# Optimization experiments

Measured on AMD Instinct MI355X. Metric: run time of the kernel, lower is better.

## Reference

```python
import jax, jax.numpy as jnp
import numpy as np

B, N, F_IN, HID, OUT, NHEADS = 16, 1024, 64, 64, 64, 4
TAXI = 512        # get_Parameter('taxi_size') from the original repo (node split point)
ALPHA = 0.2       # LeakyReLU negative slope


def setup_inputs() -> dict:
    key = jax.random.key(0)
    ks = jax.random.split(key, 8)
    x = jax.random.normal(ks[0], (B, N, F_IN), dtype=jnp.float32)
    # multiplicative binary mask (mostly ones so softmax rows are well-conditioned)
    mask = (jax.random.uniform(ks[1], (N, N)) > 0.1).astype(jnp.float32)
    s_in = 1.0 / np.sqrt(F_IN)
    s_cat = 1.0 / np.sqrt(NHEADS * HID)
    W1 = jax.random.normal(ks[2], (NHEADS, F_IN, HID), jnp.float32) * s_in
    W2 = jax.random.normal(ks[3], (NHEADS, F_IN, HID), jnp.float32) * s_in
    a = jax.random.normal(ks[4], (NHEADS, 2 * HID), jnp.float32) * 0.1
    W1o = jax.random.normal(ks[5], (NHEADS * HID, OUT), jnp.float32) * s_cat
    W2o = jax.random.normal(ks[6], (NHEADS * HID, OUT), jnp.float32) * s_cat
    ao = jax.random.normal(ks[7], (2 * OUT,), jnp.float32) * 0.1
    return dict(x=x, mask=mask, W1=W1, W2=W2, a=a, W1o=W1o, W2o=W2o, ao=ao)


def _gat_layer(x, mask, W1, W2, a, out_dim):
    # x: [B,N,F]; W1,W2: [F,out_dim]; a: [2*out_dim]
    # node-group-split linear projection (taxi nodes via W1, rest via W2)
    h = jnp.concatenate([x[:, :TAXI] @ W1, x[:, TAXI:] @ W2], axis=1)  # [B,N,O]
    A1 = h @ a[:out_dim]                 # [B,N]
    A2 = h @ a[out_dim:]                 # [B,N]
    sim = A1[:, :, None] + A2[:, None, :]  # [B,N,N] additive scores
    e = jax.nn.leaky_relu(sim, ALPHA)
    e = mask[None, :, :] * e             # multiplicative mask (as in source)
    attn = jax.nn.softmax(e, axis=-1)    # [B,N,N]  (dropout omitted: eval mode)
    h_prime = jnp.einsum('bnm,bmo->bno', attn, h)
    return jax.nn.elu(h_prime), attn


def reference(x, mask, W1, W2, a, W1o, W2o, ao):
    # input dropout omitted (eval mode)
    heads = [_gat_layer(x, mask, W1[i], W2[i], a[i], HID)[0] for i in range(NHEADS)]
    xc = jnp.concatenate(heads, axis=-1)          # [B,N,NHEADS*HID]
    out, attn = _gat_layer(xc, mask, W1o, W2o, ao, OUT)
    return out, attn
```

## Files before the change

kernel.cpp:

```cpp
#include <hip/hip_runtime.h>
#include <hip/hip_bf16.h>

#define B_      16
#define N_      1024
#define ALPHA_  0.2f

typedef __attribute__((ext_vector_type(8))) __bf16 bf16x8;
typedef __attribute__((ext_vector_type(4))) float  floatx4;

__device__ __forceinline__ float eluf(float u) { return u > 0.f ? u : __expf(u) - 1.f; }

__device__ __forceinline__ floatx4 mfma_bf16(bf16x8 a, bf16x8 b, floatx4 c) {
    return __builtin_amdgcn_mfma_f32_16x16x32_bf16(a, b, c, 0, 0, 0);
}

__device__ __forceinline__ void t_quad(const float4 a2v, const float4 ep, const float4 en,
                                       const float4 mv, const float th,
                                       const float e1p, const float e1n,
                                       float& z, float* o)
{
    float t0 = ((a2v.x > th) ? ep.x : en.x) * ((a2v.x > th) ? e1p : e1n);
    float t1 = ((a2v.y > th) ? ep.y : en.y) * ((a2v.y > th) ? e1p : e1n);
    float t2 = ((a2v.z > th) ? ep.z : en.z) * ((a2v.z > th) ? e1p : e1n);
    float t3 = ((a2v.w > th) ? ep.w : en.w) * ((a2v.w > th) ? e1p : e1n);
    t0 = (mv.x != 0.f) ? t0 : 1.f;
    t1 = (mv.y != 0.f) ? t1 : 1.f;
    t2 = (mv.z != 0.f) ? t2 : 1.f;
    t3 = (mv.w != 0.f) ? t3 : 1.f;
    z += ((t0 + t1) + (t2 + t3));
    o[0] = t0; o[1] = t1; o[2] = t2; o[3] = t3;
}

__global__ __launch_bounds__(256) void proj1_kernel(
    const float* __restrict__ x, const float* __restrict__ W1,
    const float* __restrict__ W2, const float* __restrict__ av,
    __bf16* __restrict__ h1t, float* __restrict__ A1, float* __restrict__ A2)
{
    const int tile = blockIdx.x, b = blockIdx.y, head = blockIdx.z;
    const int n0 = tile * 64;
    const float* W  = ((n0 < 512) ? W1 : W2) + head * 64 * 64;
    const float* ah = av + head * 128;

    __shared__ __align__(16) float xs[64][65];
    __shared__ __align__(16) float Wl[64][64];
    __shared__ __align__(16) float as_[128];

    const int tid = threadIdx.x;
    for (int i = 0; i < 16; ++i) {
        int idx = i * 256 + tid;
        int r = idx >> 6, f = idx & 63;
        xs[r][f] = x[(size_t)(b * N_ + n0 + r) * 64 + f];
        Wl[r][f] = W[idx];
    }
    if (tid < 128) as_[tid] = ah[tid];
    __syncthreads();

    const int r = tid >> 2, c0 = (tid & 3) * 16;
    float acc[16];
#pragma unroll
    for (int j = 0; j < 16; ++j) acc[j] = 0.f;
#pragma unroll 8
    for (int f = 0; f < 64; ++f) {
        float xv = xs[r][f];
#pragma unroll
        for (int j = 0; j < 16; ++j) acc[j] += xv * Wl[f][c0 + j];
    }

    float p1 = 0.f, p2 = 0.f;
#pragma unroll
    for (int j = 0; j < 16; ++j) {
        p1 += acc[j] * as_[c0 + j];
        p2 += acc[j] * as_[64 + c0 + j];
    }
    p1 += __shfl_xor(p1, 1); p1 += __shfl_xor(p1, 2);
    p2 += __shfl_xor(p2, 1); p2 += __shfl_xor(p2, 2);
    const int bh = head * B_ + b;
    if ((tid & 3) == 0) {
        A1[bh * N_ + n0 + r] = p1;
        A2[bh * N_ + n0 + r] = p2;
    }

    __syncthreads();
#pragma unroll
    for (int j = 0; j < 16; ++j) xs[r][c0 + j] = acc[j];
    __syncthreads();
    const int d = tid & 63, ch = tid >> 6;
    bf16x8 q0, q1;
#pragma unroll
    for (int j = 0; j < 8; ++j) q0[j] = (__bf16)xs[ch * 16 + j][d];
#pragma unroll
    for (int j = 0; j < 8; ++j) q1[j] = (__bf16)xs[ch * 16 + 8 + j][d];
    bf16x8* dst = (bf16x8*)(h1t + ((size_t)bh * 64 + d) * N_ + n0 + ch * 16);
    dst[0] = q0; dst[1] = q1;
}

__global__ __launch_bounds__(256, 4) void attn1_kernel(
    const float* __restrict__ A1g, const float* __restrict__ A2g,
    const __bf16* __restrict__ Htg, const float* __restrict__ maskg,
    __bf16* __restrict__ xc_out)
{
    const int tile = blockIdx.x, b = blockIdx.y, head = blockIdx.z;
    const int n0 = tile * 64;
    const int bh = head * B_ + b;
    const float* A1 = A1g + (size_t)bh * N_;
    const float* A2 = A2g + (size_t)bh * N_;
    const __bf16* Hglob = Htg + (size_t)bh * 64 * N_;

    __shared__ __align__(16) __bf16 ts[64][72];
    __shared__ __align__(16) __bf16 Ht[64][72];
    __shared__ __align__(16) float E2p[N_], E2n[N_], A2s[N_];
    __shared__ float invz[64];

    const int tid = threadIdx.x;
#pragma unroll
    for (int i = 0; i < 4; ++i) {
        int m = i * 256 + tid;
        float a2 = A2[m];
        A2s[m] = a2; E2p[m] = __expf(a2); E2n[m] = __expf(ALPHA_ * a2);
    }

    const int r = tid >> 2, q = tid & 3;
    const float a1r = A1[n0 + r];
    const float e1p = __expf(a1r), e1n = __expf(ALPHA_ * a1r), th = -a1r;
    const int w = tid >> 6, L = tid & 63, quad = L >> 4, lo = L & 15;

    floatx4 acc[4] = {{0,0,0,0},{0,0,0,0},{0,0,0,0},{0,0,0,0}};
    float zacc = 0.f;

    const float* mrow = maskg + (size_t)(n0 + r) * N_ + q * 16;
    const __bf16* hrow = Hglob + (size_t)r * N_ + q * 16;
    float4 pm0 = *(const float4*)(mrow);
    float4 pm1 = *(const float4*)(mrow + 4);
    float4 pm2 = *(const float4*)(mrow + 8);
    float4 pm3 = *(const float4*)(mrow + 12);
    bf16x8 ph0 = *(const bf16x8*)(hrow);
    bf16x8 ph1 = *(const bf16x8*)(hrow + 8);

    for (int mt = 0; mt < 16; ++mt) {
        float4 cm0 = pm0, cm1 = pm1, cm2 = pm2, cm3 = pm3;
        bf16x8 ch0 = ph0, ch1 = ph1;
        if (mt < 15) {
            const float* mnx = mrow + (mt + 1) * 64;
            const __bf16* hnx = hrow + (mt + 1) * 64;
            pm0 = *(const float4*)(mnx);      pm1 = *(const float4*)(mnx + 4);
            pm2 = *(const float4*)(mnx + 8);  pm3 = *(const float4*)(mnx + 12);
            ph0 = *(const bf16x8*)(hnx);      ph1 = *(const bf16x8*)(hnx + 8);
        }
        __syncthreads();
        const int mb = mt * 64 + q * 16;
        float o[16];
        t_quad(*(const float4*)&A2s[mb+0],  *(const float4*)&E2p[mb+0],  *(const float4*)&E2n[mb+0],  cm0, th, e1p, e1n, zacc, o+0);
        t_quad(*(const float4*)&A2s[mb+4],  *(const float4*)&E2p[mb+4],  *(const float4*)&E2n[mb+4],  cm1, th, e1p, e1n, zacc, o+4);
        t_quad(*(const float4*)&A2s[mb+8],  *(const float4*)&E2p[mb+8],  *(const float4*)&E2n[mb+8],  cm2, th, e1p, e1n, zacc, o+8);
        t_quad(*(const float4*)&A2s[mb+12], *(const float4*)&E2p[mb+12], *(const float4*)&E2n[mb+12], cm3, th, e1p, e1n, zacc, o+12);
        bf16x8 pk0 = {(__bf16)o[0], (__bf16)o[1], (__bf16)o[2], (__bf16)o[3],
                      (__bf16)o[4], (__bf16)o[5], (__bf16)o[6], (__bf16)o[7]};
        bf16x8 pk1 = {(__bf16)o[8], (__bf16)o[9], (__bf16)o[10], (__bf16)o[11],
                      (__bf16)o[12], (__bf16)o[13], (__bf16)o[14], (__bf16)o[15]};
        *(bf16x8*)&ts[r][q * 16]     = pk0;
        *(bf16x8*)&ts[r][q * 16 + 8] = pk1;
        *(bf16x8*)&Ht[r][q * 16]     = ch0;
        *(bf16x8*)&Ht[r][q * 16 + 8] = ch1;
        __syncthreads();
#pragma unroll
        for (int c = 0; c < 2; ++c) {
            bf16x8 af = *(bf16x8*)&ts[16 * w + lo][c * 32 + quad * 8];
#pragma unroll
            for (int t = 0; t < 4; ++t) {
                bf16x8 bv = *(bf16x8*)&Ht[16 * t + lo][c * 32 + quad * 8];
                acc[t] = mfma_bf16(af, bv, acc[t]);
            }
        }
    }

    zacc += __shfl_xor(zacc, 1);
    zacc += __shfl_xor(zacc, 2);
    if (q == 0) invz[r] = 1.f / zacc;
    __syncthreads();

#pragma unroll
    for (int t = 0; t < 4; ++t)
#pragma unroll
        for (int i = 0; i < 4; ++i) {
            const int n = 16 * w + quad * 4 + i;
            ts[n][16 * t + lo] = (__bf16)eluf(acc[t][i] * invz[n]);
        }
    __syncthreads();
#pragma unroll
    for (int i = 0; i < 2; ++i) {
        int cid = i * 256 + tid;
        int row = cid >> 3, c8 = (cid & 7) * 8;
        bf16x8 v = *(bf16x8*)&ts[row][c8];
        *(bf16x8*)(xc_out + ((size_t)(b * N_ + n0 + row)) * 256 + head * 64 + c8) = v;
    }
}

__global__ __launch_bounds__(256) void attn2_kernel(
    const float* __restrict__ A1g, const float* __restrict__ A2g,
    const __bf16* __restrict__ Htg, const float* __restrict__ maskg,
    float* __restrict__ out_f, float* __restrict__ attn_f)
{
    const int tile = blockIdx.x, b = blockIdx.y;
    const int n0 = tile * 64;
    const float* A1 = A1g + (size_t)b * N_;
    const float* A2 = A2g + (size_t)b * N_;
    const __bf16* Hglob = Htg + (size_t)b * 64 * N_;

    __shared__ __align__(16) __bf16 ts[64][72];
    __shared__ __align__(16) __bf16 Ht[64][72];
    __shared__ __align__(16) float E2p[N_], E2n[N_], A2s[N_];
    __shared__ float invz[64], E1pl[64], E1nl[64], A1sl[64];

    const int tid = threadIdx.x;
#pragma unroll
    for (int i = 0; i < 4; ++i) {
        int m = i * 256 + tid;
        float a2 = A2[m];
        A2s[m] = a2; E2p[m] = __expf(a2); E2n[m] = __expf(ALPHA_ * a2);
    }

    const int r = tid >> 2, q = tid & 3;
    const float a1r = A1[n0 + r];
    const float e1p = __expf(a1r), e1n = __expf(ALPHA_ * a1r), th = -a1r;
    if (q == 0) { E1pl[r] = e1p; E1nl[r] = e1n; A1sl[r] = a1r; }
    const int w = tid >> 6, L = tid & 63, quad = L >> 4, lo = L & 15;

    floatx4 acc[4] = {{0,0,0,0},{0,0,0,0},{0,0,0,0},{0,0,0,0}};
    float zacc = 0.f;

    const float* mrow = maskg + (size_t)(n0 + r) * N_ + q * 16;
    const __bf16* hrow = Hglob + (size_t)r * N_ + q * 16;
    float4 pm0 = *(const float4*)(mrow);
    float4 pm1 = *(const float4*)(mrow + 4);
    float4 pm2 = *(const float4*)(mrow + 8);
    float4 pm3 = *(const float4*)(mrow + 12);
    bf16x8 ph0 = *(const bf16x8*)(hrow);
    bf16x8 ph1 = *(const bf16x8*)(hrow + 8);

    for (int mt = 0; mt < 16; ++mt) {
        float4 cm0 = pm0, cm1 = pm1, cm2 = pm2, cm3 = pm3;
        bf16x8 ch0 = ph0, ch1 = ph1;
        if (mt < 15) {
            const float* mnx = mrow + (mt + 1) * 64;
            const __bf16* hnx = hrow + (mt + 1) * 64;
            pm0 = *(const float4*)(mnx);      pm1 = *(const float4*)(mnx + 4);
            pm2 = *(const float4*)(mnx + 8);  pm3 = *(const float4*)(mnx + 12);
            ph0 = *(const bf16x8*)(hnx);      ph1 = *(const bf16x8*)(hnx + 8);
        }
        __syncthreads();
        const int mb = mt * 64 + q * 16;
        float o[16];
        t_quad(*(const float4*)&A2s[mb+0],  *(const float4*)&E2p[mb+0],  *(const float4*)&E2n[mb+0],  cm0, th, e1p, e1n, zacc, o+0);
        t_quad(*(const float4*)&A2s[mb+4],  *(const float4*)&E2p[mb+4],  *(const float4*)&E2n[mb+4],  cm1, th, e1p, e1n, zacc, o+4);
        t_quad(*(const float4*)&A2s[mb+8],  *(const float4*)&E2p[mb+8],  *(const float4*)&E2n[mb+8],  cm2, th, e1p, e1n, zacc, o+8);
        t_quad(*(const float4*)&A2s[mb+12], *(const float4*)&E2p[mb+12], *(const float4*)&E2n[mb+12], cm3, th, e1p, e1n, zacc, o+12);
        bf16x8 pk0 = {(__bf16)o[0], (__bf16)o[1], (__bf16)o[2], (__bf16)o[3],
                      (__bf16)o[4], (__bf16)o[5], (__bf16)o[6], (__bf16)o[7]};
        bf16x8 pk1 = {(__bf16)o[8], (__bf16)o[9], (__bf16)o[10], (__bf16)o[11],
                      (__bf16)o[12], (__bf16)o[13], (__bf16)o[14], (__bf16)o[15]};
        *(bf16x8*)&ts[r][q * 16]     = pk0;
        *(bf16x8*)&ts[r][q * 16 + 8] = pk1;
        *(bf16x8*)&Ht[r][q * 16]     = ch0;
        *(bf16x8*)&Ht[r][q * 16 + 8] = ch1;
        __syncthreads();
#pragma unroll
        for (int c = 0; c < 2; ++c) {
            bf16x8 af = *(bf16x8*)&ts[16 * w + lo][c * 32 + quad * 8];
#pragma unroll
            for (int t = 0; t < 4; ++t) {
                bf16x8 bv = *(bf16x8*)&Ht[16 * t + lo][c * 32 + quad * 8];
                acc[t] = mfma_bf16(af, bv, acc[t]);
            }
        }
    }

    zacc += __shfl_xor(zacc, 1);
    zacc += __shfl_xor(zacc, 2);
    if (q == 0) invz[r] = 1.f / zacc;
    __syncthreads();

#pragma unroll
    for (int t = 0; t < 4; ++t)
#pragma unroll
        for (int i = 0; i < 4; ++i) {
            const int n = 16 * w + quad * 4 + i;
            out_f[((size_t)(b * N_ + n0 + n)) * 64 + 16 * t + lo] = eluf(acc[t][i] * invz[n]);
        }

    const float4 a2v = *(const float4*)&A2s[tid * 4];
    const float4 epv = *(const float4*)&E2p[tid * 4];
    const float4 env = *(const float4*)&E2n[tid * 4];
#pragma unroll 2
    for (int i = 0; i < 64; ++i) {
        const float e1pr = E1pl[i], e1nr = E1nl[i], thr = -A1sl[i], iz = invz[i];
        float4 mv = *(const float4*)(maskg + (size_t)(n0 + i) * N_ + tid * 4);
        float4 res;
        res.x = ((mv.x != 0.f) ? ((a2v.x > thr) ? epv.x * e1pr : env.x * e1nr) : 1.f) * iz;
        res.y = ((mv.y != 0.f) ? ((a2v.y > thr) ? epv.y * e1pr : env.y * e1nr) : 1.f) * iz;
        res.z = ((mv.z != 0.f) ? ((a2v.z > thr) ? epv.z * e1pr : env.z * e1nr) : 1.f) * iz;
        res.w = ((mv.w != 0.f) ? ((a2v.w > thr) ? epv.w * e1pr : env.w * e1nr) : 1.f) * iz;
        *(float4*)(attn_f + ((size_t)(b * N_ + n0 + i)) * N_ + tid * 4) = res;
    }
}

__global__ __launch_bounds__(256) void proj2_kernel(
    const __bf16* __restrict__ xcb, const float* __restrict__ W1o,
    const float* __restrict__ W2o, const float* __restrict__ ao,
    __bf16* __restrict__ h2t, float* __restrict__ A1o, float* __restrict__ A2o)
{
    const int tile = blockIdx.x, b = blockIdx.y;
    const int n0 = tile * 64;
    const float* W = (n0 < 512) ? W1o : W2o;

    __shared__ __align__(16) __bf16 xs[64][264];
    __shared__ __align__(16) __bf16 Wt[64][264];
    __shared__ __align__(16) float as_[128];

    const int tid = threadIdx.x;
    if (tid < 128) as_[tid] = ao[tid];

#pragma unroll
    for (int i = 0; i < 8; ++i) {
        int idx = i * 256 + tid;
        int row = idx >> 5, c = (idx & 31) * 8;
        *(bf16x8*)&xs[row][c] =
            *(const bf16x8*)(xcb + ((size_t)(b * N_ + n0 + row)) * 256 + c);
    }
#pragma unroll
    for (int i = 0; i < 16; ++i) {
        int idx = i * 256 + tid;
        int k = idx >> 4, n4 = (idx & 15) * 4;
        float4 wv = *(const float4*)(W + (size_t)k * 64 + n4);
        Wt[n4 + 0][k] = (__bf16)wv.x;
        Wt[n4 + 1][k] = (__bf16)wv.y;
        Wt[n4 + 2][k] = (__bf16)wv.z;
        Wt[n4 + 3][k] = (__bf16)wv.w;
    }
    __syncthreads();

    const int w = tid >> 6, L = tid & 63, quad = L >> 4, lo = L & 15;
    floatx4 acc[4] = {{0,0,0,0},{0,0,0,0},{0,0,0,0},{0,0,0,0}};
#pragma unroll
    for (int kc = 0; kc < 8; ++kc) {
        bf16x8 af = *(bf16x8*)&xs[16 * w + lo][kc * 32 + quad * 8];
#pragma unroll
        for (int t = 0; t < 4; ++t) {
            bf16x8 bv = *(bf16x8*)&Wt[16 * t + lo][kc * 32 + quad * 8];
            acc[t] = mfma_bf16(af, bv, acc[t]);
        }
    }

    float p1[4] = {0, 0, 0, 0}, p2[4] = {0, 0, 0, 0};
#pragma unroll
    for (int t = 0; t < 4; ++t) {
        float a1w = as_[16 * t + lo], a2w = as_[64 + 16 * t + lo];
#pragma unroll
        for (int i = 0; i < 4; ++i) { p1[i] += acc[t][i] * a1w; p2[i] += acc[t][i] * a2w; }
    }
#pragma unroll
    for (int s = 1; s < 16; s <<= 1)
#pragma unroll
        for (int i = 0; i < 4; ++i) {
            p1[i] += __shfl_xor(p1[i], s);
            p2[i] += __shfl_xor(p2[i], s);
        }
    if (lo == 0) {
#pragma unroll
        for (int i = 0; i < 4; ++i) {
            int n = 16 * w + quad * 4 + i;
            A1o[b * N_ + n0 + n] = p1[i];
            A2o[b * N_ + n0 + n] = p2[i];
        }
    }

    __syncthreads();
#pragma unroll
    for (int t = 0; t < 4; ++t)
#pragma unroll
        for (int i = 0; i < 4; ++i)
            xs[16 * w + quad * 4 + i][16 * t + lo] = (__bf16)acc[t][i];
    __syncthreads();
    const int d = tid & 63, ch = tid >> 6;
    bf16x8 v0, v1;
#pragma unroll
    for (int j = 0; j < 8; ++j) v0[j] = xs[ch * 16 + j][d];
#pragma unroll
    for (int j = 0; j < 8; ++j) v1[j] = xs[ch * 16 + 8 + j][d];
    bf16x8* dst = (bf16x8*)(h2t + ((size_t)b * 64 + d) * N_ + n0 + ch * 16);
    dst[0] = v0; dst[1] = v1;
}

extern "C" void kernel_launch(void* const* d_in, const int* in_sizes, int n_in,
                              void* d_out, int out_size, void* d_ws, size_t ws_size,
                              hipStream_t stream)
{
    const float* x    = (const float*)d_in[0];
    const float* mask = (const float*)d_in[1];
    const float* W1   = (const float*)d_in[2];
    const float* W2   = (const float*)d_in[3];
    const float* a    = (const float*)d_in[4];
    const float* W1o  = (const float*)d_in[5];
    const float* W2o  = (const float*)d_in[6];
    const float* ao   = (const float*)d_in[7];

    float* out      = (float*)d_out;
    float* attn_out = out + (size_t)B_ * N_ * 64;

    float*  ws  = (float*)d_ws;
    float*  A1  = ws;
    float*  A2  = A1 + 65536;
    float*  A1o = A2 + 65536;
    float*  A2o = A1o + 16384;
    __bf16* h1t = (__bf16*)(A2o + 16384);
    __bf16* h2t = h1t + 4194304;
    __bf16* xcb = h2t + 1048576;

    proj1_kernel<<<dim3(16, 16, 4), 256, 0, stream>>>(x, W1, W2, a, h1t, A1, A2);
    attn1_kernel<<<dim3(16, 16, 4), 256, 0, stream>>>(A1, A2, h1t, mask, xcb);
    proj2_kernel<<<dim3(16, 16, 1), 256, 0, stream>>>(xcb, W1o, W2o, ao, h2t, A1o, A2o);
    attn2_kernel<<<dim3(16, 16, 1), 256, 0, stream>>>(A1o, A2o, h2t, mask, out, attn_out);
}
```

Measured before the change: 177.4 us.

## Use bf16 MFMA in proj1 and shrink attn2 row tiles for more blocks

proj1 now stages x and a transposed W in shared memory as bf16 and computes the projection with 16x16x32 bf16 MFMA instead of scalar fp32 FMAs. The A1/A2 attention logits are reduced across 16 lanes with shuffles. attn2 goes from 64-row tiles to 16-row tiles, launching 1024 blocks instead of 256 so the final layer and its attention-matrix write fill the GPU. The cost is reduced precision in the first projection and less reuse of the H tile per block in attn2.

```diff
diff --git a/kernel.cpp b/kernel.cpp
--- a/kernel.cpp
+++ b/kernel.cpp
@@ -6,6 +6,7 @@
 #define ALPHA_  0.2f
 
 typedef __attribute__((ext_vector_type(8))) __bf16 bf16x8;
+typedef __attribute__((ext_vector_type(4))) __bf16 bf16x4;
 typedef __attribute__((ext_vector_type(4))) float  floatx4;
 
 __device__ __forceinline__ float eluf(float u) { return u > 0.f ? u : __expf(u) - 1.f; }
@@ -41,57 +42,76 @@
     const float* W  = ((n0 < 512) ? W1 : W2) + head * 64 * 64;
     const float* ah = av + head * 128;
 
-    __shared__ __align__(16) float xs[64][65];
-    __shared__ __align__(16) float Wl[64][64];
+    __shared__ __align__(16) __bf16 xs[64][72];
+    __shared__ __align__(16) __bf16 Wt[64][72];
     __shared__ __align__(16) float as_[128];
 
     const int tid = threadIdx.x;
-    for (int i = 0; i < 16; ++i) {
+    if (tid < 128) as_[tid] = ah[tid];
+#pragma unroll
+    for (int i = 0; i < 4; ++i) {
         int idx = i * 256 + tid;
-        int r = idx >> 6, f = idx & 63;
-        xs[r][f] = x[(size_t)(b * N_ + n0 + r) * 64 + f];
-        Wl[r][f] = W[idx];
-    }
-    if (tid < 128) as_[tid] = ah[tid];
-    __syncthreads();
-
-    const int r = tid >> 2, c0 = (tid & 3) * 16;
-    float acc[16];
-#pragma unroll
-    for (int j = 0; j < 16; ++j) acc[j] = 0.f;
-#pragma unroll 8
-    for (int f = 0; f < 64; ++f) {
-        float xv = xs[r][f];
-#pragma unroll
-        for (int j = 0; j < 16; ++j) acc[j] += xv * Wl[f][c0 + j];
-    }
-
-    float p1 = 0.f, p2 = 0.f;
-#pragma unroll
-    for (int j = 0; j < 16; ++j) {
-        p1 += acc[j] * as_[c0 + j];
-        p2 += acc[j] * as_[64 + c0 + j];
-    }
-    p1 += __shfl_xor(p1, 1); p1 += __shfl_xor(p1, 2);
-    p2 += __shfl_xor(p2, 1); p2 += __shfl_xor(p2, 2);
+        int r = idx >> 4, c = (idx & 15) * 4;
+        float4 v = *(const float4*)(x + ((size_t)(b * N_ + n0 + r)) * 64 + c);
+        xs[r][c+0] = (__bf16)v.x; xs[r][c+1] = (__bf16)v.y;
+        xs[r][c+2] = (__bf16)v.z; xs[r][c+3] = (__bf16)v.w;
+        float4 wv = *(const float4*)(W + (size_t)r * 64 + c);
+        Wt[c+0][r] = (__bf16)wv.x; Wt[c+1][r] = (__bf16)wv.y;
+        Wt[c+2][r] = (__bf16)wv.z; Wt[c+3][r] = (__bf16)wv.w;
+    }
+    __syncthreads();
+
+    const int w = tid >> 6, L = tid & 63, quad = L >> 4, lo = L & 15;
+    floatx4 acc[4] = {{0,0,0,0},{0,0,0,0},{0,0,0,0},{0,0,0,0}};
+#pragma unroll
+    for (int kc = 0; kc < 2; ++kc) {
+        bf16x8 af = *(bf16x8*)&xs[16 * w + lo][kc * 32 + quad * 8];
+#pragma unroll
+        for (int t = 0; t < 4; ++t) {
+            bf16x8 bv = *(bf16x8*)&Wt[16 * t + lo][kc * 32 + quad * 8];
+            acc[t] = mfma_bf16(af, bv, acc[t]);
+        }
+    }
+
+    float p1[4] = {0, 0, 0, 0}, p2[4] = {0, 0, 0, 0};
+#pragma unroll
+    for (int t = 0; t < 4; ++t) {
+        float a1w = as_[16 * t + lo], a2w = as_[64 + 16 * t + lo];
+#pragma unroll
+        for (int i = 0; i < 4; ++i) { p1[i] += acc[t][i] * a1w; p2[i] += acc[t][i] * a2w; }
+    }
+#pragma unroll
+    for (int s = 1; s < 16; s <<= 1)
+#pragma unroll
+        for (int i = 0; i < 4; ++i) {
+            p1[i] += __shfl_xor(p1[i], s);
+            p2[i] += __shfl_xor(p2[i], s);
+        }
     const int bh = head * B_ + b;
-    if ((tid & 3) == 0) {
-        A1[bh * N_ + n0 + r] = p1;
-        A2[bh * N_ + n0 + r] = p2;
-    }
-
-    __syncthreads();
-#pragma unroll
-    for (int j = 0; j < 16; ++j) xs[r][c0 + j] = acc[j];
+    if (lo == 0) {
+#pragma unroll
+        for (int i = 0; i < 4; ++i) {
+            int n = 16 * w + quad * 4 + i;
+            A1[bh * N_ + n0 + n] = p1[i];
+            A2[bh * N_ + n0 + n] = p2[i];
+        }
+    }
+
+    __syncthreads();
+#pragma unroll
+    for (int t = 0; t < 4; ++t)
+#pragma unroll
+        for (int i = 0; i < 4; ++i)
+            xs[16 * w + quad * 4 + i][16 * t + lo] = (__bf16)acc[t][i];
     __syncthreads();
     const int d = tid & 63, ch = tid >> 6;
-    bf16x8 q0, q1;
-#pragma unroll
-    for (int j = 0; j < 8; ++j) q0[j] = (__bf16)xs[ch * 16 + j][d];
-#pragma unroll
-    for (int j = 0; j < 8; ++j) q1[j] = (__bf16)xs[ch * 16 + 8 + j][d];
+    bf16x8 v0, v1;
+#pragma unroll
+    for (int j = 0; j < 8; ++j) v0[j] = xs[ch * 16 + j][d];
+#pragma unroll
+    for (int j = 0; j < 8; ++j) v1[j] = xs[ch * 16 + 8 + j][d];
     bf16x8* dst = (bf16x8*)(h1t + ((size_t)bh * 64 + d) * N_ + n0 + ch * 16);
-    dst[0] = q0; dst[1] = q1;
+    dst[0] = v0; dst[1] = v1;
 }
 
 __global__ __launch_bounds__(256, 4) void attn1_kernel(
@@ -201,15 +221,15 @@
     float* __restrict__ out_f, float* __restrict__ attn_f)
 {
     const int tile = blockIdx.x, b = blockIdx.y;
-    const int n0 = tile * 64;
+    const int n0 = tile * 16;
     const float* A1 = A1g + (size_t)b * N_;
     const float* A2 = A2g + (size_t)b * N_;
     const __bf16* Hglob = Htg + (size_t)b * 64 * N_;
 
-    __shared__ __align__(16) __bf16 ts[64][72];
+    __shared__ __align__(16) __bf16 ts[16][72];
     __shared__ __align__(16) __bf16 Ht[64][72];
     __shared__ __align__(16) float E2p[N_], E2n[N_], A2s[N_];
-    __shared__ float invz[64], E1pl[64], E1nl[64], A1sl[64];
+    __shared__ float invz[16], E1pl[16], E1nl[16], A1sl[16];
 
     const int tid = threadIdx.x;
 #pragma unroll
@@ -219,79 +239,66 @@
         A2s[m] = a2; E2p[m] = __expf(a2); E2n[m] = __expf(ALPHA_ * a2);
     }
 
-    const int r = tid >> 2, q = tid & 3;
+    const int r = tid >> 4, q = tid & 15;
     const float a1r = A1[n0 + r];
     const float e1p = __expf(a1r), e1n = __expf(ALPHA_ * a1r), th = -a1r;
     if (q == 0) { E1pl[r] = e1p; E1nl[r] = e1n; A1sl[r] = a1r; }
+    const int dr = tid >> 2, dq = tid & 3;
     const int w = tid >> 6, L = tid & 63, quad = L >> 4, lo = L & 15;
 
-    floatx4 acc[4] = {{0,0,0,0},{0,0,0,0},{0,0,0,0},{0,0,0,0}};
+    floatx4 acc = {0, 0, 0, 0};
     float zacc = 0.f;
 
-    const float* mrow = maskg + (size_t)(n0 + r) * N_ + q * 16;
-    const __bf16* hrow = Hglob + (size_t)r * N_ + q * 16;
-    float4 pm0 = *(const float4*)(mrow);
-    float4 pm1 = *(const float4*)(mrow + 4);
-    float4 pm2 = *(const float4*)(mrow + 8);
-    float4 pm3 = *(const float4*)(mrow + 12);
+    const float* mrow = maskg + (size_t)(n0 + r) * N_ + q * 4;
+    const __bf16* hrow = Hglob + (size_t)dr * N_ + dq * 16;
+    float4 pm = *(const float4*)(mrow);
     bf16x8 ph0 = *(const bf16x8*)(hrow);
     bf16x8 ph1 = *(const bf16x8*)(hrow + 8);
 
     for (int mt = 0; mt < 16; ++mt) {
-        float4 cm0 = pm0, cm1 = pm1, cm2 = pm2, cm3 = pm3;
+        float4 cm = pm;
         bf16x8 ch0 = ph0, ch1 = ph1;
         if (mt < 15) {
-            const float* mnx = mrow + (mt + 1) * 64;
-            const __bf16* hnx = hrow + (mt + 1) * 64;
-            pm0 = *(const float4*)(mnx);      pm1 = *(const float4*)(mnx + 4);
-            pm2 = *(const float4*)(mnx + 8);  pm3 = *(const float4*)(mnx + 12);
-            ph0 = *(const bf16x8*)(hnx);      ph1 = *(const bf16x8*)(hnx + 8);
+            pm  = *(const float4*)(mrow + (mt + 1) * 64);
+            ph0 = *(const bf16x8*)(hrow + (mt + 1) * 64);
+            ph1 = *(const bf16x8*)(hrow + (mt + 1) * 64 + 8);
         }
         __syncthreads();
-        const int mb = mt * 64 + q * 16;
-        float o[16];
-        t_quad(*(const float4*)&A2s[mb+0],  *(const float4*)&E2p[mb+0],  *(const float4*)&E2n[mb+0],  cm0, th, e1p, e1n, zacc, o+0);
-        t_quad(*(const float4*)&A2s[mb+4],  *(const float4*)&E2p[mb+4],  *(const float4*)&E2n[mb+4],  cm1, th, e1p, e1n, zacc, o+4);
-        t_quad(*(const float4*)&A2s[mb+8],  *(const float4*)&E2p[mb+8],  *(const float4*)&E2n[mb+8],  cm2, th, e1p, e1n, zacc, o+8);
-        t_quad(*(const float4*)&A2s[mb+12], *(const float4*)&E2p[mb+12], *(const float4*)&E2n[mb+12], cm3, th, e1p, e1n, zacc, o+12);
-        bf16x8 pk0 = {(__bf16)o[0], (__bf16)o[1], (__bf16)o[2], (__bf16)o[3],
-                      (__bf16)o[4], (__bf16)o[5], (__bf16)o[6], (__bf16)o[7]};
-        bf16x8 pk1 = {(__bf16)o[8], (__bf16)o[9], (__bf16)o[10], (__bf16)o[11],
-                      (__bf16)o[12], (__bf16)o[13], (__bf16)o[14], (__bf16)o[15]};
-        *(bf16x8*)&ts[r][q * 16]     = pk0;
-        *(bf16x8*)&ts[r][q * 16 + 8] = pk1;
-        *(bf16x8*)&Ht[r][q * 16]     = ch0;
-        *(bf16x8*)&Ht[r][q * 16 + 8] = ch1;
+        const int mb = mt * 64 + q * 4;
+        float o[4];
+        t_quad(*(const float4*)&A2s[mb], *(const float4*)&E2p[mb],
+               *(const float4*)&E2n[mb], cm, th, e1p, e1n, zacc, o);
+        bf16x4 pk = {(__bf16)o[0], (__bf16)o[1], (__bf16)o[2], (__bf16)o[3]};
+        *(bf16x4*)&ts[r][q * 4] = pk;
+        *(bf16x8*)&Ht[dr][dq * 16]     = ch0;
+        *(bf16x8*)&Ht[dr][dq * 16 + 8] = ch1;
         __syncthreads();
 #pragma unroll
         for (int c = 0; c < 2; ++c) {
-            bf16x8 af = *(bf16x8*)&ts[16 * w + lo][c * 32 + quad * 8];
-#pragma unroll
-            for (int t = 0; t < 4; ++t) {
-                bf16x8 bv = *(bf16x8*)&Ht[16 * t + lo][c * 32 + quad * 8];
-                acc[t] = mfma_bf16(af, bv, acc[t]);
-            }
+            bf16x8 af = *(bf16x8*)&ts[lo][c * 32 + quad * 8];
+            bf16x8 bv = *(bf16x8*)&Ht[16 * w + lo][c * 32 + quad * 8];
+            acc = mfma_bf16(af, bv, acc);
         }
     }
 
     zacc += __shfl_xor(zacc, 1);
     zacc += __shfl_xor(zacc, 2);
+    zacc += __shfl_xor(zacc, 4);
+    zacc += __shfl_xor(zacc, 8);
     if (q == 0) invz[r] = 1.f / zacc;
     __syncthreads();
 
 #pragma unroll
-    for (int t = 0; t < 4; ++t)
-#pragma unroll
-        for (int i = 0; i < 4; ++i) {
-            const int n = 16 * w + quad * 4 + i;
-            out_f[((size_t)(b * N_ + n0 + n)) * 64 + 16 * t + lo] = eluf(acc[t][i] * invz[n]);
-        }
+    for (int i = 0; i < 4; ++i) {
+        const int n = quad * 4 + i;
+        out_f[((size_t)(b * N_ + n0 + n)) * 64 + 16 * w + lo] = eluf(acc[i] * invz[n]);
+    }
 
     const float4 a2v = *(const float4*)&A2s[tid * 4];
     const float4 epv = *(const float4*)&E2p[tid * 4];
     const float4 env = *(const float4*)&E2n[tid * 4];
-#pragma unroll 2
-    for (int i = 0; i < 64; ++i) {
+#pragma unroll 4
+    for (int i = 0; i < 16; ++i) {
         const float e1pr = E1pl[i], e1nr = E1nl[i], thr = -A1sl[i], iz = invz[i];
         float4 mv = *(const float4*)(maskg + (size_t)(n0 + i) * N_ + tid * 4);
         float4 res;
@@ -418,5 +425,5 @@
     proj1_kernel<<<dim3(16, 16, 4), 256, 0, stream>>>(x, W1, W2, a, h1t, A1, A2);
     attn1_kernel<<<dim3(16, 16, 4), 256, 0, stream>>>(A1, A2, h1t, mask, xcb);
     proj2_kernel<<<dim3(16, 16, 1), 256, 0, stream>>>(xcb, W1o, W2o, ao, h2t, A1o, A2o);
-    attn2_kernel<<<dim3(16, 16, 1), 256, 0, stream>>>(A1o, A2o, h2t, mask, out, attn_out);
-}
+    attn2_kernel<<<dim3(64, 16, 1), 256, 0, stream>>>(A1o, A2o, h2t, mask, out, attn_out);
+}
```

New measurement: 168.5 us. 1.05x faster.
